# Optimization experiments

Measured on AMD Instinct MI355X. Metric: run time of the kernel, lower is better.

Reference implementation:

```python
import jax, jax.numpy as jnp
import numpy as np

N = 100000          # nodes
E = 3200000         # edges (avg degree 32)
D_IN = 64           # node_feature_dim
D_EMB = 128         # config.GNN_EMBEDDING_DIM
D_HID = 256         # config.RNN_HIDDEN_DIM


def setup_inputs() -> dict:
    key = jax.random.key(0)
    ks = jax.random.split(key, 12)
    s = 0.05
    return {
        "node_features": jax.random.normal(ks[0], (N, D_IN), jnp.float32),
        "edge_attr": jax.random.normal(ks[1], (E, 1), jnp.float32),
        "hidden_state": jax.random.normal(ks[2], (1, D_HID), jnp.float32),
        "W_enc": jax.random.normal(ks[3], (D_EMB, D_IN), jnp.float32) * s,
        "b_enc": jnp.zeros((D_EMB,), jnp.float32),
        "W_gcn": jax.random.normal(ks[4], (D_EMB, D_EMB), jnp.float32) * s,
        "b_gcn": jnp.zeros((D_EMB,), jnp.float32),
        "W_ih": jax.random.normal(ks[5], (3 * D_HID, D_EMB), jnp.float32) * s,
        "W_hh": jax.random.normal(ks[6], (3 * D_HID, D_HID), jnp.float32) * s,
        "b_ih": jax.random.normal(ks[7], (3 * D_HID,), jnp.float32) * s,
        "b_hh": jax.random.normal(ks[8], (3 * D_HID,), jnp.float32) * s,
        "edge_index": jax.random.randint(ks[9], (2, E), 0, N, jnp.int64),
    }


def reference(node_features, edge_attr, hidden_state, W_enc, b_enc, W_gcn,
              b_gcn, W_ih, W_hh, b_ih, b_hh, edge_index):
    n = node_features.shape[0]
    # Linear encoder + ReLU
    x = jax.nn.relu(node_features @ W_enc.T + b_enc)
    # GCNConv (PyG default): x' = D^-1/2 (A+I) D^-1/2 (x W^T) + b
    xw = x @ W_gcn.T
    loops = jnp.arange(n, dtype=edge_index.dtype)
    src = jnp.concatenate([edge_index[0], loops])
    dst = jnp.concatenate([edge_index[1], loops])
    deg = jax.ops.segment_sum(jnp.ones(src.shape, xw.dtype), dst, num_segments=n)
    dinv = jnp.where(deg > 0, jax.lax.rsqrt(deg), 0.0)
    norm = dinv[src] * dinv[dst]  # [E+N]
    agg = jax.ops.segment_sum(norm[:, None] * xw[src], dst, num_segments=n)
    g = jax.nn.relu(agg + b_gcn)
    agent = g[0:1, :]  # [1, D_EMB]
    # GRUCell
    gi = agent @ W_ih.T + b_ih
    gh = hidden_state @ W_hh.T + b_hh
    i_r, i_z, i_n = jnp.split(gi, 3, axis=1)
    h_r, h_z, h_n = jnp.split(gh, 3, axis=1)
    r = jax.nn.sigmoid(i_r + h_r)
    z = jax.nn.sigmoid(i_z + h_z)
    nn_ = jnp.tanh(i_n + r * h_n)
    return (1.0 - z) * nn_ + z * hidden_state
```

## Files before the change

kernel.cpp:

```cpp
#include <hip/hip_runtime.h>
#include <hip/hip_bf16.h>
#include <cstddef>

typedef __hip_bfloat16 bf16;

#define SB   1024
#define SL   32
#define CAP  256
#define TILE 64

__device__ __forceinline__ float ldf(const void* p, int isf32, long long i) {
    if (isf32) return ((const float*)p)[i];
    return __bfloat162float(((const bf16*)p)[i]);
}

__device__ __forceinline__ void detect(const void* ei, const void* wenc,
                                       int& is64, int& isf32) {
    int l = threadIdx.x & 63;
    int hi = (l < 16) ? ((const int*)ei)[2 * l + 1] : 0;
    unsigned long long any_hi = __ballot(hi != 0);
    unsigned short u = ((const unsigned short*)wenc)[l];
    unsigned short ex = (u >> 7) & 0xFF;
    unsigned long long any_big = __ballot(ex >= 137);
    is64  = (any_hi == 0ull) ? 1 : 0;
    isf32 = (any_big != 0ull) ? 1 : 0;
}

__device__ __forceinline__ void build_list(const int* __restrict__ cnts,
                                           const int* __restrict__ srcs,
                                           int* ls_src, int* ls_slot,
                                           int* sh_cnt, int* sh_tot,
                                           int& cnt, int& tot) {
    const int t = threadIdx.x;
    if (t == 0) { *sh_cnt = 0; *sh_tot = 0; }
    __syncthreads();
    for (int i = t; i < SB; i += 256) {
        int c = cnts[i];
        if (c > 0) {
            atomicAdd(sh_tot, c);
            int cc = min(c, SL);
            int base = atomicAdd(sh_cnt, cc);
            for (int j = 0; j < cc; j++) {
                int pos = base + j;
                if (pos < CAP) {
                    ls_src[pos]  = srcs[i * SL + j];
                    ls_slot[pos] = i * SL + j;
                }
            }
        }
    }
    __syncthreads();
    cnt = min(*sh_cnt, CAP);
    tot = *sh_tot;
}

__global__ void __launch_bounds__(256) k_scan(
        const void* __restrict__ ei, long long E,
        const void* __restrict__ wenc,
        const void* __restrict__ hid,
        const void* __restrict__ Whh, const void* __restrict__ bhh,
        int* __restrict__ cnts, int* __restrict__ srcs,
        int* __restrict__ degs, float* __restrict__ gh) {
    __shared__ float red[4];
    __shared__ int lc;
    __shared__ int ls[SL];
    int is64, isf32;
    detect(ei, wenc, is64, isf32);
    const int b = blockIdx.x;
    const int t = threadIdx.x;
    if (b < SB) {
        if (t == 0) lc = 0;
        if (t < SL) degs[b * SL + t] = 0;
        __syncthreads();
        const long long NT = (long long)SB * 256;
        if ((E & 1) == 0) {
            const long long P = E >> 1;
            for (long long p = (long long)b * 256 + t; p < P; p += NT) {
                int d0, d1;
                if (is64) {
                    longlong2 dd = ((const longlong2*)ei)[P + p];
                    d0 = (int)dd.x; d1 = (int)dd.y;
                } else {
                    int2 dd = ((const int2*)ei)[P + p];
                    d0 = dd.x; d1 = dd.y;
                }
                if (d0 == 0) {
                    int q = atomicAdd(&lc, 1);
                    if (q < SL) ls[q] = (int)(is64 ? ((const long long*)ei)[2*p]
                                                   : (long long)((const int*)ei)[2*p]);
                }
                if (d1 == 0) {
                    int q = atomicAdd(&lc, 1);
                    if (q < SL) ls[q] = (int)(is64 ? ((const long long*)ei)[2*p+1]
                                                   : (long long)((const int*)ei)[2*p+1]);
                }
            }
        } else {
            for (long long e = (long long)b * 256 + t; e < E; e += NT) {
                int d = is64 ? (int)((const long long*)ei)[E + e] : ((const int*)ei)[E + e];
                if (d == 0) {
                    int q = atomicAdd(&lc, 1);
                    if (q < SL) ls[q] = (int)(is64 ? ((const long long*)ei)[e]
                                                   : (long long)((const int*)ei)[e]);
                }
            }
        }
        __syncthreads();
        int c = lc;
        if (t == 0) cnts[b] = c;
        if (t < min(c, SL)) srcs[b * SL + t] = ls[t];
    } else {
        int j = b - SB;
        float p = ldf(Whh, isf32, (long long)j * 256 + t) * ldf(hid, isf32, t);
        #pragma unroll
        for (int off = 32; off > 0; off >>= 1) p += __shfl_down(p, off);
        if ((t & 63) == 0) red[t >> 6] = p;
        __syncthreads();
        if (t == 0) gh[j] = red[0] + red[1] + red[2] + red[3] + ldf(bhh, isf32, j);
    }
}

__global__ void __launch_bounds__(256) k_deg(
        const void* __restrict__ ei, long long E,
        const void* __restrict__ wenc,
        const int* __restrict__ cnts, const int* __restrict__ srcs,
        int* __restrict__ degs) {
    __shared__ int ls_src[CAP];
    __shared__ int ls_slot[CAP];
    __shared__ int sh_cnt, sh_tot;
    int is64, isf32;
    detect(ei, wenc, is64, isf32);
    (void)isf32;
    int cnt, tot;
    build_list(cnts, srcs, ls_src, ls_slot, &sh_cnt, &sh_tot, cnt, tot);
    const int b = blockIdx.x;
    const int t = threadIdx.x;
    const long long NT = (long long)gridDim.x * 256;
    if ((E & 1) == 0) {
        const long long P = E >> 1;
        for (long long p = (long long)b * 256 + t; p < P; p += NT) {
            int d0, d1;
            if (is64) {
                longlong2 dd = ((const longlong2*)ei)[P + p];
                d0 = (int)dd.x; d1 = (int)dd.y;
            } else {
                int2 dd = ((const int2*)ei)[P + p];
                d0 = dd.x; d1 = dd.y;
            }
            for (int j = 0; j < cnt; j++) {
                if (ls_src[j] == d0) atomicAdd(&degs[ls_slot[j]], 1);
                if (ls_src[j] == d1) atomicAdd(&degs[ls_slot[j]], 1);
            }
        }
    } else {
        for (long long e = (long long)b * 256 + t; e < E; e += NT) {
            int d = is64 ? (int)((const long long*)ei)[E + e] : ((const int*)ei)[E + e];
            for (int j = 0; j < cnt; j++)
                if (ls_src[j] == d) atomicAdd(&degs[ls_slot[j]], 1);
        }
    }
}

__global__ void __launch_bounds__(256) k_gru(
        const void* __restrict__ ei,
        const void* __restrict__ nf,
        const void* __restrict__ Wenc, const void* __restrict__ benc,
        const void* __restrict__ Wgcn, const void* __restrict__ bgcn,
        const void* __restrict__ hid,
        const void* __restrict__ Wih,  const void* __restrict__ bih,
        const int* __restrict__ cnts, const int* __restrict__ srcs,
        const int* __restrict__ degs, const float* __restrict__ gh,
        void* __restrict__ out) {
    __shared__ int   ls_src[CAP];
    __shared__ int   ls_slot[CAP];
    __shared__ int   sh_cnt, sh_tot;
    __shared__ float norm_s[CAP + 1];
    __shared__ __align__(16) float xs[TILE][64];
    __shared__ float part[2][128];
    __shared__ float ysum_s[128];
    __shared__ float g0_s[128];
    __shared__ float red[3];
    int is64, isf32;
    detect(ei, Wenc, is64, isf32);
    (void)is64;
    int cnt, tot;
    build_list(cnts, srcs, ls_src, ls_slot, &sh_cnt, &sh_tot, cnt, tot);
    const int t = threadIdx.x;
    const int lane = t & 63, wid = t >> 6;
    const int td = t & 127, hf = t >> 7;

    const int deg0 = tot + 1;
    const float r0 = rsqrtf((float)deg0);
    for (int i = t; i < cnt; i += 256)
        norm_s[i] = rsqrtf((float)(degs[ls_slot[i]] + 1)) * r0;
    if (t == 0) norm_s[cnt] = 1.0f / (float)deg0;
    const int total = cnt + 1;

    float4 wreg[16];
    if (isf32) {
        const float4* wr = (const float4*)((const float*)Wenc + (size_t)td * 64);
        #pragma unroll
        for (int k = 0; k < 16; k++) wreg[k] = wr[k];
    }
    const float be = ldf(benc, isf32, td);
    float ysum_acc = 0.0f;
    __syncthreads();

    for (int base = 0; base < total; base += TILE) {
        const int tn = min(TILE, total - base);
        for (int idx = t; idx < tn * 64; idx += 256) {
            int j = idx >> 6, c = idx & 63;
            int node = base + j;
            int s = (node < cnt) ? ls_src[node] : 0;
            xs[j][c] = ldf(nf, isf32, (long long)s * 64 + c);
        }
        __syncthreads();
        if (isf32) {
            for (int jj = hf; jj < tn; jj += 4) {
                const int ok2 = (jj + 2 < tn);
                const float4* xa = (const float4*)xs[jj];
                const float4* xb = (const float4*)xs[ok2 ? jj + 2 : jj];
                float aa = 0.0f, ab = 0.0f;
                #pragma unroll
                for (int k = 0; k < 16; k++) {
                    float4 va = xa[k], vb = xb[k], w = wreg[k];
                    aa += w.x*va.x + w.y*va.y + w.z*va.z + w.w*va.w;
                    ab += w.x*vb.x + w.y*vb.y + w.z*vb.z + w.w*vb.w;
                }
                float ya = fmaxf(aa + be, 0.0f);
                float yb = fmaxf(ab + be, 0.0f);
                ysum_acc += norm_s[base + jj] * ya
                          + (ok2 ? norm_s[base + jj + 2] * yb : 0.0f);
            }
        } else {
            for (int j = hf; j < tn; j += 2) {
                float acc = 0.0f;
                for (int k = 0; k < 64; k++)
                    acc += ldf(Wenc, 0, (long long)td * 64 + k) * xs[j][k];
                ysum_acc += norm_s[base + j] * fmaxf(acc + be, 0.0f);
            }
        }
        __syncthreads();
    }
    part[hf][td] = ysum_acc;
    __syncthreads();
    if (t < 128) ysum_s[t] = part[0][t] + part[1][t];
    __syncthreads();

    {
        float acc = 0.0f;
        if (isf32) {
            const float4* gr = (const float4*)((const float*)Wgcn
                                + (size_t)td * 128 + (size_t)hf * 64);
            const float* ys = ysum_s + hf * 64;
            #pragma unroll
            for (int k = 0; k < 16; k++) {
                float4 v = gr[k];
                acc += v.x*ys[4*k] + v.y*ys[4*k+1] + v.z*ys[4*k+2] + v.w*ys[4*k+3];
            }
        } else {
            for (int k = 0; k < 64; k++)
                acc += ldf(Wgcn, 0, (long long)td * 128 + hf * 64 + k)
                     * ysum_s[hf * 64 + k];
        }
        part[hf][td] = acc;
    }
    __syncthreads();
    if (t < 128)
        g0_s[t] = fmaxf(part[0][t] + part[1][t] + ldf(bgcn, isf32, t), 0.0f);
    __syncthreads();

    const int b = blockIdx.x;
    if (wid < 3) {
        long long j = (long long)wid * 256 + b;
        float a;
        if (isf32) {
            const float* wr = (const float*)Wih + (size_t)j * 128;
            a = wr[lane] * g0_s[lane] + wr[64 + lane] * g0_s[64 + lane];
        } else {
            a = ldf(Wih, 0, j * 128 + lane)      * g0_s[lane]
              + ldf(Wih, 0, j * 128 + 64 + lane) * g0_s[64 + lane];
        }
        #pragma unroll
        for (int off = 32; off > 0; off >>= 1) a += __shfl_down(a, off);
        if (lane == 0) red[wid] = a;
    }
    __syncthreads();
    if (t == 0) {
        float rr = 1.0f / (1.0f + expf(-(red[0] + ldf(bih, isf32, b)       + gh[b])));
        float zz = 1.0f / (1.0f + expf(-(red[1] + ldf(bih, isf32, 256 + b) + gh[256 + b])));
        float nn = tanhf(red[2] + ldf(bih, isf32, 512 + b) + rr * gh[512 + b]);
        float hh = ldf(hid, isf32, b);
        float val = (1.0f - zz) * nn + zz * hh;
        if (isf32) ((float*)out)[b] = val;
        else       ((bf16*)out)[b]  = __float2bfloat16(val);
    }
}

extern "C" void kernel_launch(void* const* d_in, const int* in_sizes, int n_in,
                              void* d_out, int out_size, void* d_ws, size_t ws_size,
                              hipStream_t stream) {
    const void* nf   = d_in[0];
    const void* hid  = d_in[2];
    const void* Wenc = d_in[3];
    const void* benc = d_in[4];
    const void* Wgcn = d_in[5];
    const void* bgcn = d_in[6];
    const void* Wih  = d_in[7];
    const void* Whh  = d_in[8];
    const void* bih  = d_in[9];
    const void* bhh  = d_in[10];
    const void* ei   = d_in[11];
    long long E = in_sizes[11] / 2;

    int*   cnts = (int*)d_ws;
    int*   srcs = cnts + SB;
    int*   degs = srcs + SB * SL;
    float* gh   = (float*)(degs + SB * SL);

    k_scan<<<SB + 768, 256, 0, stream>>>(ei, E, Wenc, hid, Whh, bhh,
                                         cnts, srcs, degs, gh);
    k_deg<<<2048, 256, 0, stream>>>(ei, E, Wenc, cnts, srcs, degs);
    k_gru<<<256, 256, 0, stream>>>(ei, nf, Wenc, benc, Wgcn, bgcn, hid,
                                   Wih, bih, cnts, srcs, degs, gh, d_out);
}
```

Before: 146.2 us.

## Prefetch weights and neighbour features into cache, move W_hh GEMV into GRU kernel

Adds prefetch blocks to the scan kernel that read all weight matrices so they sit in L2/MALL before the final kernel needs them. Adds an extra block to the degree kernel that touches node-0's neighbour feature rows for the same reason. Moves the hidden-state GEMV from the scan kernel into the GRU kernel and doubles the scan grid. This shortens the latency-bound last kernel, at the cost of extra blocks and redundant loads in the earlier kernels.

```diff
diff --git a/kernel.cpp b/kernel.cpp
--- a/kernel.cpp
+++ b/kernel.cpp
@@ -4,7 +4,8 @@
 
 typedef __hip_bfloat16 bf16;
 
-#define SB   1024
+#define SB   2048
+#define WB   64
 #define SL   32
 #define CAP  256
 #define TILE 64
@@ -56,86 +57,100 @@
 
 __global__ void __launch_bounds__(256) k_scan(
         const void* __restrict__ ei, long long E,
-        const void* __restrict__ wenc,
-        const void* __restrict__ hid,
-        const void* __restrict__ Whh, const void* __restrict__ bhh,
+        const void* __restrict__ Wenc,
+        const void* __restrict__ Wgcn,
+        const void* __restrict__ Wih, const void* __restrict__ Whh,
         int* __restrict__ cnts, int* __restrict__ srcs,
-        int* __restrict__ degs, float* __restrict__ gh) {
-    __shared__ float red[4];
+        int* __restrict__ degs) {
     __shared__ int lc;
     __shared__ int ls[SL];
     int is64, isf32;
-    detect(ei, wenc, is64, isf32);
+    detect(ei, Wenc, is64, isf32);
     const int b = blockIdx.x;
     const int t = threadIdx.x;
-    if (b < SB) {
-        if (t == 0) lc = 0;
-        if (t < SL) degs[b * SL + t] = 0;
-        __syncthreads();
-        const long long NT = (long long)SB * 256;
-        if ((E & 1) == 0) {
-            const long long P = E >> 1;
-            for (long long p = (long long)b * 256 + t; p < P; p += NT) {
-                int d0, d1;
-                if (is64) {
-                    longlong2 dd = ((const longlong2*)ei)[P + p];
-                    d0 = (int)dd.x; d1 = (int)dd.y;
-                } else {
-                    int2 dd = ((const int2*)ei)[P + p];
-                    d0 = dd.x; d1 = dd.y;
-                }
-                if (d0 == 0) {
-                    int q = atomicAdd(&lc, 1);
-                    if (q < SL) ls[q] = (int)(is64 ? ((const long long*)ei)[2*p]
-                                                   : (long long)((const int*)ei)[2*p]);
-                }
-                if (d1 == 0) {
-                    int q = atomicAdd(&lc, 1);
-                    if (q < SL) ls[q] = (int)(is64 ? ((const long long*)ei)[2*p+1]
-                                                   : (long long)((const int*)ei)[2*p+1]);
-                }
-            }
-        } else {
-            for (long long e = (long long)b * 256 + t; e < E; e += NT) {
-                int d = is64 ? (int)((const long long*)ei)[E + e] : ((const int*)ei)[E + e];
-                if (d == 0) {
-                    int q = atomicAdd(&lc, 1);
-                    if (q < SL) ls[q] = (int)(is64 ? ((const long long*)ei)[e]
-                                                   : (long long)((const int*)ei)[e]);
-                }
-            }
-        }
-        __syncthreads();
-        int c = lc;
-        if (t == 0) cnts[b] = c;
-        if (t < min(c, SL)) srcs[b * SL + t] = ls[t];
+    if (b < WB) {
+        const long long esz = isf32 ? 4 : 2;
+        const void* arrs[4]  = { Wenc, Wgcn, Wih, Whh };
+        const long long el[4] = { 128 * 64, 128 * 128, 768 * 128, 768 * 256 };
+        int acc = 0;
+        for (int a = 0; a < 4; a++) {
+            const char* pb = (const char*)arrs[a];
+            const long long nb = el[a] * esz;
+            for (long long off = ((long long)b * 256 + t) * 16;
+                 off + 16 <= nb; off += (long long)WB * 256 * 16) {
+                int4 v = *(const int4*)(pb + off);
+                acc += v.x + v.y + v.z + v.w;
+            }
+        }
+        asm volatile("" :: "v"(acc));
+        return;
+    }
+    const int sb = b - WB;
+    if (t == 0) lc = 0;
+    if (t < SL) degs[sb * SL + t] = 0;
+    __syncthreads();
+    const long long NT = (long long)SB * 256;
+    if ((E & 1) == 0) {
+        const long long P = E >> 1;
+        for (long long p = (long long)sb * 256 + t; p < P; p += NT) {
+            int d0, d1;
+            if (is64) {
+                longlong2 dd = ((const longlong2*)ei)[P + p];
+                d0 = (int)dd.x; d1 = (int)dd.y;
+            } else {
+                int2 dd = ((const int2*)ei)[P + p];
+                d0 = dd.x; d1 = dd.y;
+            }
+            if (d0 == 0) {
+                int q = atomicAdd(&lc, 1);
+                if (q < SL) ls[q] = (int)(is64 ? ((const long long*)ei)[2*p]
+                                               : (long long)((const int*)ei)[2*p]);
+            }
+            if (d1 == 0) {
+                int q = atomicAdd(&lc, 1);
+                if (q < SL) ls[q] = (int)(is64 ? ((const long long*)ei)[2*p+1]
+                                               : (long long)((const int*)ei)[2*p+1]);
+            }
+        }
     } else {
-        int j = b - SB;
-        float p = ldf(Whh, isf32, (long long)j * 256 + t) * ldf(hid, isf32, t);
-        #pragma unroll
-        for (int off = 32; off > 0; off >>= 1) p += __shfl_down(p, off);
-        if ((t & 63) == 0) red[t >> 6] = p;
-        __syncthreads();
-        if (t == 0) gh[j] = red[0] + red[1] + red[2] + red[3] + ldf(bhh, isf32, j);
-    }
+        for (long long e = (long long)sb * 256 + t; e < E; e += NT) {
+            int d = is64 ? (int)((const long long*)ei)[E + e] : ((const int*)ei)[E + e];
+            if (d == 0) {
+                int q = atomicAdd(&lc, 1);
+                if (q < SL) ls[q] = (int)(is64 ? ((const long long*)ei)[e]
+                                               : (long long)((const int*)ei)[e]);
+            }
+        }
+    }
+    __syncthreads();
+    int c = lc;
+    if (t == 0) cnts[sb] = c;
+    if (t < min(c, SL)) srcs[sb * SL + t] = ls[t];
 }
 
 __global__ void __launch_bounds__(256) k_deg(
         const void* __restrict__ ei, long long E,
         const void* __restrict__ wenc,
+        const void* __restrict__ nf,
         const int* __restrict__ cnts, const int* __restrict__ srcs,
-        int* __restrict__ degs) {
+        int* __restrict__ degs, int DB) {
     __shared__ int ls_src[CAP];
     __shared__ int ls_slot[CAP];
     __shared__ int sh_cnt, sh_tot;
     int is64, isf32;
     detect(ei, wenc, is64, isf32);
-    (void)isf32;
     int cnt, tot;
     build_list(cnts, srcs, ls_src, ls_slot, &sh_cnt, &sh_tot, cnt, tot);
     const int b = blockIdx.x;
     const int t = threadIdx.x;
-    const long long NT = (long long)gridDim.x * 256;
+    if (b >= DB) {
+        float s = 0.0f;
+        for (int idx = t; idx < cnt * 64; idx += 256)
+            s += ldf(nf, isf32, (long long)ls_src[idx >> 6] * 64 + (idx & 63));
+        asm volatile("" :: "v"(s));
+        return;
+    }
+    const long long NT = (long long)DB * 256;
     if ((E & 1) == 0) {
         const long long P = E >> 1;
         for (long long p = (long long)b * 256 + t; p < P; p += NT) {
@@ -168,18 +183,19 @@
         const void* __restrict__ Wgcn, const void* __restrict__ bgcn,
         const void* __restrict__ hid,
         const void* __restrict__ Wih,  const void* __restrict__ bih,
+        const void* __restrict__ Whh,  const void* __restrict__ bhh,
         const int* __restrict__ cnts, const int* __restrict__ srcs,
-        const int* __restrict__ degs, const float* __restrict__ gh,
-        void* __restrict__ out) {
+        const int* __restrict__ degs, void* __restrict__ out) {
     __shared__ int   ls_src[CAP];
     __shared__ int   ls_slot[CAP];
     __shared__ int   sh_cnt, sh_tot;
     __shared__ float norm_s[CAP + 1];
+    __shared__ float hid_s[256];
     __shared__ __align__(16) float xs[TILE][64];
     __shared__ float part[2][128];
     __shared__ float ysum_s[128];
     __shared__ float g0_s[128];
-    __shared__ float red[3];
+    __shared__ float red_ih[3], red_hh[3];
     int is64, isf32;
     detect(ei, Wenc, is64, isf32);
     (void)is64;
@@ -188,6 +204,7 @@
     const int t = threadIdx.x;
     const int lane = t & 63, wid = t >> 6;
     const int td = t & 127, hf = t >> 7;
+    hid_s[t] = ldf(hid, isf32, t);
 
     const int deg0 = tot + 1;
     const float r0 = rsqrtf((float)deg0);
@@ -273,24 +290,37 @@
     const int b = blockIdx.x;
     if (wid < 3) {
         long long j = (long long)wid * 256 + b;
-        float a;
+        float aih, ahh = 0.0f;
         if (isf32) {
             const float* wr = (const float*)Wih + (size_t)j * 128;
-            a = wr[lane] * g0_s[lane] + wr[64 + lane] * g0_s[64 + lane];
+            aih = wr[lane] * g0_s[lane] + wr[64 + lane] * g0_s[64 + lane];
+            const float* hr = (const float*)Whh + (size_t)j * 256;
+            #pragma unroll
+            for (int q = 0; q < 4; q++)
+                ahh += hr[q * 64 + lane] * hid_s[q * 64 + lane];
         } else {
-            a = ldf(Wih, 0, j * 128 + lane)      * g0_s[lane]
-              + ldf(Wih, 0, j * 128 + 64 + lane) * g0_s[64 + lane];
+            aih = ldf(Wih, 0, j * 128 + lane)      * g0_s[lane]
+                + ldf(Wih, 0, j * 128 + 64 + lane) * g0_s[64 + lane];
+            #pragma unroll
+            for (int q = 0; q < 4; q++)
+                ahh += ldf(Whh, 0, j * 256 + q * 64 + lane) * hid_s[q * 64 + lane];
         }
         #pragma unroll
-        for (int off = 32; off > 0; off >>= 1) a += __shfl_down(a, off);
-        if (lane == 0) red[wid] = a;
+        for (int off = 32; off > 0; off >>= 1) {
+            aih += __shfl_down(aih, off);
+            ahh += __shfl_down(ahh, off);
+        }
+        if (lane == 0) { red_ih[wid] = aih; red_hh[wid] = ahh; }
     }
     __syncthreads();
     if (t == 0) {
-        float rr = 1.0f / (1.0f + expf(-(red[0] + ldf(bih, isf32, b)       + gh[b])));
-        float zz = 1.0f / (1.0f + expf(-(red[1] + ldf(bih, isf32, 256 + b) + gh[256 + b])));
-        float nn = tanhf(red[2] + ldf(bih, isf32, 512 + b) + rr * gh[512 + b]);
-        float hh = ldf(hid, isf32, b);
+        float gh0 = red_hh[0] + ldf(bhh, isf32, b);
+        float gh1 = red_hh[1] + ldf(bhh, isf32, 256 + b);
+        float gh2 = red_hh[2] + ldf(bhh, isf32, 512 + b);
+        float rr = 1.0f / (1.0f + expf(-(red_ih[0] + ldf(bih, isf32, b)       + gh0)));
+        float zz = 1.0f / (1.0f + expf(-(red_ih[1] + ldf(bih, isf32, 256 + b) + gh1)));
+        float nn = tanhf(red_ih[2] + ldf(bih, isf32, 512 + b) + rr * gh2);
+        float hh = hid_s[b];
         float val = (1.0f - zz) * nn + zz * hh;
         if (isf32) ((float*)out)[b] = val;
         else       ((bf16*)out)[b]  = __float2bfloat16(val);
@@ -313,14 +343,14 @@
     const void* ei   = d_in[11];
     long long E = in_sizes[11] / 2;
 
-    int*   cnts = (int*)d_ws;
-    int*   srcs = cnts + SB;
-    int*   degs = srcs + SB * SL;
-    float* gh   = (float*)(degs + SB * SL);
-
-    k_scan<<<SB + 768, 256, 0, stream>>>(ei, E, Wenc, hid, Whh, bhh,
-                                         cnts, srcs, degs, gh);
-    k_deg<<<2048, 256, 0, stream>>>(ei, E, Wenc, cnts, srcs, degs);
+    int* cnts = (int*)d_ws;
+    int* srcs = cnts + SB;
+    int* degs = srcs + SB * SL;
+
+    const int DB = 2048;
+    k_scan<<<WB + SB, 256, 0, stream>>>(ei, E, Wenc, Wgcn, Wih, Whh,
+                                        cnts, srcs, degs);
+    k_deg<<<DB + 1, 256, 0, stream>>>(ei, E, Wenc, nf, cnts, srcs, degs, DB);
     k_gru<<<256, 256, 0, stream>>>(ei, nf, Wenc, benc, Wgcn, bgcn, hid,
-                                   Wih, bih, cnts, srcs, degs, gh, d_out);
-}
+                                   Wih, bih, Whh, bhh, cnts, srcs, degs, d_out);
+}
```

Measured after the change: 153.8 us. 1.05x slower.

## Fuse scan, degree and GRU stages into one cooperative persistent kernel

Applied to the files above, without the earlier changes.

Replaces the three-kernel pipeline with a single cooperative kernel. Each block scans the destination indices once, keeps them in registers, and uses global atomic counters with spin-wait barriers to publish agent-neighbor lists and their degrees before the first GRU blocks run the gather and GRU step. The W_hh matvec moves into the GRU blocks, and the original three-kernel path is kept as a fallback if the cooperative launch fails. This removes launch gaps and the second full read of the edge list, at the cost of grid-wide spin barriers and an occupancy-limited grid size.

```diff
diff --git a/kernel.cpp b/kernel.cpp
--- a/kernel.cpp
+++ b/kernel.cpp
@@ -4,10 +4,14 @@
 
 typedef __hip_bfloat16 bf16;
 
-#define SB   1024
-#define SL   32
-#define CAP  256
-#define TILE 64
+#define CAP   256
+#define PMAX  16
+#define GRUB  256
+#define SL    32
+#define TILE  64
+#define SB3   1024
+#define DB3   2048
+#define MAGIC 0x9E3779B1
 
 __device__ __forceinline__ float ldf(const void* p, int isf32, long long i) {
     if (isf32) return ((const float*)p)[i];
@@ -26,176 +30,38 @@
     isf32 = (any_big != 0ull) ? 1 : 0;
 }
 
-__device__ __forceinline__ void build_list(const int* __restrict__ cnts,
-                                           const int* __restrict__ srcs,
-                                           int* ls_src, int* ls_slot,
-                                           int* sh_cnt, int* sh_tot,
-                                           int& cnt, int& tot) {
-    const int t = threadIdx.x;
-    if (t == 0) { *sh_cnt = 0; *sh_tot = 0; }
-    __syncthreads();
-    for (int i = t; i < SB; i += 256) {
-        int c = cnts[i];
-        if (c > 0) {
-            atomicAdd(sh_tot, c);
-            int cc = min(c, SL);
-            int base = atomicAdd(sh_cnt, cc);
-            for (int j = 0; j < cc; j++) {
-                int pos = base + j;
-                if (pos < CAP) {
-                    ls_src[pos]  = srcs[i * SL + j];
-                    ls_slot[pos] = i * SL + j;
-                }
-            }
-        }
-    }
-    __syncthreads();
-    cnt = min(*sh_cnt, CAP);
-    tot = *sh_tot;
-}
-
-__global__ void __launch_bounds__(256) k_scan(
-        const void* __restrict__ ei, long long E,
-        const void* __restrict__ wenc,
-        const void* __restrict__ hid,
-        const void* __restrict__ Whh, const void* __restrict__ bhh,
-        int* __restrict__ cnts, int* __restrict__ srcs,
-        int* __restrict__ degs, float* __restrict__ gh) {
-    __shared__ float red[4];
-    __shared__ int lc;
-    __shared__ int ls[SL];
-    int is64, isf32;
-    detect(ei, wenc, is64, isf32);
-    const int b = blockIdx.x;
-    const int t = threadIdx.x;
-    if (b < SB) {
-        if (t == 0) lc = 0;
-        if (t < SL) degs[b * SL + t] = 0;
-        __syncthreads();
-        const long long NT = (long long)SB * 256;
-        if ((E & 1) == 0) {
-            const long long P = E >> 1;
-            for (long long p = (long long)b * 256 + t; p < P; p += NT) {
-                int d0, d1;
-                if (is64) {
-                    longlong2 dd = ((const longlong2*)ei)[P + p];
-                    d0 = (int)dd.x; d1 = (int)dd.y;
-                } else {
-                    int2 dd = ((const int2*)ei)[P + p];
-                    d0 = dd.x; d1 = dd.y;
-                }
-                if (d0 == 0) {
-                    int q = atomicAdd(&lc, 1);
-                    if (q < SL) ls[q] = (int)(is64 ? ((const long long*)ei)[2*p]
-                                                   : (long long)((const int*)ei)[2*p]);
-                }
-                if (d1 == 0) {
-                    int q = atomicAdd(&lc, 1);
-                    if (q < SL) ls[q] = (int)(is64 ? ((const long long*)ei)[2*p+1]
-                                                   : (long long)((const int*)ei)[2*p+1]);
-                }
-            }
-        } else {
-            for (long long e = (long long)b * 256 + t; e < E; e += NT) {
-                int d = is64 ? (int)((const long long*)ei)[E + e] : ((const int*)ei)[E + e];
-                if (d == 0) {
-                    int q = atomicAdd(&lc, 1);
-                    if (q < SL) ls[q] = (int)(is64 ? ((const long long*)ei)[e]
-                                                   : (long long)((const int*)ei)[e]);
-                }
-            }
-        }
-        __syncthreads();
-        int c = lc;
-        if (t == 0) cnts[b] = c;
-        if (t < min(c, SL)) srcs[b * SL + t] = ls[t];
-    } else {
-        int j = b - SB;
-        float p = ldf(Whh, isf32, (long long)j * 256 + t) * ldf(hid, isf32, t);
-        #pragma unroll
-        for (int off = 32; off > 0; off >>= 1) p += __shfl_down(p, off);
-        if ((t & 63) == 0) red[t >> 6] = p;
-        __syncthreads();
-        if (t == 0) gh[j] = red[0] + red[1] + red[2] + red[3] + ldf(bhh, isf32, j);
-    }
-}
-
-__global__ void __launch_bounds__(256) k_deg(
-        const void* __restrict__ ei, long long E,
-        const void* __restrict__ wenc,
-        const int* __restrict__ cnts, const int* __restrict__ srcs,
-        int* __restrict__ degs) {
-    __shared__ int ls_src[CAP];
-    __shared__ int ls_slot[CAP];
-    __shared__ int sh_cnt, sh_tot;
-    int is64, isf32;
-    detect(ei, wenc, is64, isf32);
-    (void)isf32;
-    int cnt, tot;
-    build_list(cnts, srcs, ls_src, ls_slot, &sh_cnt, &sh_tot, cnt, tot);
-    const int b = blockIdx.x;
-    const int t = threadIdx.x;
-    const long long NT = (long long)gridDim.x * 256;
-    if ((E & 1) == 0) {
-        const long long P = E >> 1;
-        for (long long p = (long long)b * 256 + t; p < P; p += NT) {
-            int d0, d1;
-            if (is64) {
-                longlong2 dd = ((const longlong2*)ei)[P + p];
-                d0 = (int)dd.x; d1 = (int)dd.y;
-            } else {
-                int2 dd = ((const int2*)ei)[P + p];
-                d0 = dd.x; d1 = dd.y;
-            }
-            for (int j = 0; j < cnt; j++) {
-                if (ls_src[j] == d0) atomicAdd(&degs[ls_slot[j]], 1);
-                if (ls_src[j] == d1) atomicAdd(&degs[ls_slot[j]], 1);
-            }
-        }
-    } else {
-        for (long long e = (long long)b * 256 + t; e < E; e += NT) {
-            int d = is64 ? (int)((const long long*)ei)[E + e] : ((const int*)ei)[E + e];
-            for (int j = 0; j < cnt; j++)
-                if (ls_src[j] == d) atomicAdd(&degs[ls_slot[j]], 1);
-        }
-    }
-}
-
-__global__ void __launch_bounds__(256) k_gru(
-        const void* __restrict__ ei,
+__device__ __forceinline__ int aload(int* p) {
+    return __hip_atomic_load(p, __ATOMIC_RELAXED, __HIP_MEMORY_SCOPE_AGENT);
+}
+__device__ __forceinline__ void backoff() {
+    #pragma unroll
+    for (int i = 0; i < 8; i++) __builtin_amdgcn_s_sleep(7);
+}
+
+struct GruSmem {
+    float norm_s[CAP + 1];
+    float hid_s[256];
+    __align__(16) float xs[TILE][64];
+    float part[2][128];
+    float ysum_s[128];
+    float g0_s[128];
+    float red_ih[3], red_hh[3];
+};
+
+__device__ __forceinline__ void gather_gru(
+        const int* __restrict__ ls_src, GruSmem* sm, int cnt, int isf32, int ob,
         const void* __restrict__ nf,
         const void* __restrict__ Wenc, const void* __restrict__ benc,
         const void* __restrict__ Wgcn, const void* __restrict__ bgcn,
         const void* __restrict__ hid,
         const void* __restrict__ Wih,  const void* __restrict__ bih,
-        const int* __restrict__ cnts, const int* __restrict__ srcs,
-        const int* __restrict__ degs, const float* __restrict__ gh,
+        const void* __restrict__ Whh,  const void* __restrict__ bhh,
         void* __restrict__ out) {
-    __shared__ int   ls_src[CAP];
-    __shared__ int   ls_slot[CAP];
-    __shared__ int   sh_cnt, sh_tot;
-    __shared__ float norm_s[CAP + 1];
-    __shared__ __align__(16) float xs[TILE][64];
-    __shared__ float part[2][128];
-    __shared__ float ysum_s[128];
-    __shared__ float g0_s[128];
-    __shared__ float red[3];
-    int is64, isf32;
-    detect(ei, Wenc, is64, isf32);
-    (void)is64;
-    int cnt, tot;
-    build_list(cnts, srcs, ls_src, ls_slot, &sh_cnt, &sh_tot, cnt, tot);
     const int t = threadIdx.x;
     const int lane = t & 63, wid = t >> 6;
     const int td = t & 127, hf = t >> 7;
-
-    const int deg0 = tot + 1;
-    const float r0 = rsqrtf((float)deg0);
-    for (int i = t; i < cnt; i += 256)
-        norm_s[i] = rsqrtf((float)(degs[ls_slot[i]] + 1)) * r0;
-    if (t == 0) norm_s[cnt] = 1.0f / (float)deg0;
+    sm->hid_s[t] = ldf(hid, isf32, t);
     const int total = cnt + 1;
-
     float4 wreg[16];
     if (isf32) {
         const float4* wr = (const float4*)((const float*)Wenc + (size_t)td * 64);
@@ -205,21 +71,20 @@
     const float be = ldf(benc, isf32, td);
     float ysum_acc = 0.0f;
     __syncthreads();
-
     for (int base = 0; base < total; base += TILE) {
         const int tn = min(TILE, total - base);
         for (int idx = t; idx < tn * 64; idx += 256) {
             int j = idx >> 6, c = idx & 63;
             int node = base + j;
             int s = (node < cnt) ? ls_src[node] : 0;
-            xs[j][c] = ldf(nf, isf32, (long long)s * 64 + c);
+            sm->xs[j][c] = ldf(nf, isf32, (long long)s * 64 + c);
         }
         __syncthreads();
         if (isf32) {
             for (int jj = hf; jj < tn; jj += 4) {
                 const int ok2 = (jj + 2 < tn);
-                const float4* xa = (const float4*)xs[jj];
-                const float4* xb = (const float4*)xs[ok2 ? jj + 2 : jj];
+                const float4* xa = (const float4*)sm->xs[jj];
+                const float4* xb = (const float4*)sm->xs[ok2 ? jj + 2 : jj];
                 float aa = 0.0f, ab = 0.0f;
                 #pragma unroll
                 for (int k = 0; k < 16; k++) {
@@ -229,30 +94,29 @@
                 }
                 float ya = fmaxf(aa + be, 0.0f);
                 float yb = fmaxf(ab + be, 0.0f);
-                ysum_acc += norm_s[base + jj] * ya
-                          + (ok2 ? norm_s[base + jj + 2] * yb : 0.0f);
+                ysum_acc += sm->norm_s[base + jj] * ya
+                          + (ok2 ? sm->norm_s[base + jj + 2] * yb : 0.0f);
             }
         } else {
             for (int j = hf; j < tn; j += 2) {
                 float acc = 0.0f;
                 for (int k = 0; k < 64; k++)
-                    acc += ldf(Wenc, 0, (long long)td * 64 + k) * xs[j][k];
-                ysum_acc += norm_s[base + j] * fmaxf(acc + be, 0.0f);
+                    acc += ldf(Wenc, 0, (long long)td * 64 + k) * sm->xs[j][k];
+                ysum_acc += sm->norm_s[base + j] * fmaxf(acc + be, 0.0f);
             }
         }
         __syncthreads();
     }
-    part[hf][td] = ysum_acc;
-    __syncthreads();
-    if (t < 128) ysum_s[t] = part[0][t] + part[1][t];
-    __syncthreads();
-
+    sm->part[hf][td] = ysum_acc;
+    __syncthreads();
+    if (t < 128) sm->ysum_s[t] = sm->part[0][t] + sm->part[1][t];
+    __syncthreads();
     {
         float acc = 0.0f;
         if (isf32) {
             const float4* gr = (const float4*)((const float*)Wgcn
                                 + (size_t)td * 128 + (size_t)hf * 64);
-            const float* ys = ysum_s + hf * 64;
+            const float* ys = sm->ysum_s + hf * 64;
             #pragma unroll
             for (int k = 0; k < 16; k++) {
                 float4 v = gr[k];
@@ -261,40 +125,343 @@
         } else {
             for (int k = 0; k < 64; k++)
                 acc += ldf(Wgcn, 0, (long long)td * 128 + hf * 64 + k)
-                     * ysum_s[hf * 64 + k];
-        }
-        part[hf][td] = acc;
+                     * sm->ysum_s[hf * 64 + k];
+        }
+        sm->part[hf][td] = acc;
     }
     __syncthreads();
     if (t < 128)
-        g0_s[t] = fmaxf(part[0][t] + part[1][t] + ldf(bgcn, isf32, t), 0.0f);
-    __syncthreads();
-
-    const int b = blockIdx.x;
+        sm->g0_s[t] = fmaxf(sm->part[0][t] + sm->part[1][t]
+                            + ldf(bgcn, isf32, t), 0.0f);
+    __syncthreads();
     if (wid < 3) {
-        long long j = (long long)wid * 256 + b;
-        float a;
+        long long j = (long long)wid * 256 + ob;
+        float aih, ahh = 0.0f;
         if (isf32) {
             const float* wr = (const float*)Wih + (size_t)j * 128;
-            a = wr[lane] * g0_s[lane] + wr[64 + lane] * g0_s[64 + lane];
+            aih = wr[lane] * sm->g0_s[lane] + wr[64 + lane] * sm->g0_s[64 + lane];
+            const float* hr = (const float*)Whh + (size_t)j * 256;
+            #pragma unroll
+            for (int q = 0; q < 4; q++)
+                ahh += hr[q * 64 + lane] * sm->hid_s[q * 64 + lane];
         } else {
-            a = ldf(Wih, 0, j * 128 + lane)      * g0_s[lane]
-              + ldf(Wih, 0, j * 128 + 64 + lane) * g0_s[64 + lane];
+            aih = ldf(Wih, 0, j * 128 + lane)      * sm->g0_s[lane]
+                + ldf(Wih, 0, j * 128 + 64 + lane) * sm->g0_s[64 + lane];
+            #pragma unroll
+            for (int q = 0; q < 4; q++)
+                ahh += ldf(Whh, 0, j * 256 + q * 64 + lane) * sm->hid_s[q * 64 + lane];
         }
         #pragma unroll
-        for (int off = 32; off > 0; off >>= 1) a += __shfl_down(a, off);
-        if (lane == 0) red[wid] = a;
+        for (int off = 32; off > 0; off >>= 1) {
+            aih += __shfl_down(aih, off);
+            ahh += __shfl_down(ahh, off);
+        }
+        if (lane == 0) { sm->red_ih[wid] = aih; sm->red_hh[wid] = ahh; }
     }
     __syncthreads();
     if (t == 0) {
-        float rr = 1.0f / (1.0f + expf(-(red[0] + ldf(bih, isf32, b)       + gh[b])));
-        float zz = 1.0f / (1.0f + expf(-(red[1] + ldf(bih, isf32, 256 + b) + gh[256 + b])));
-        float nn = tanhf(red[2] + ldf(bih, isf32, 512 + b) + rr * gh[512 + b]);
-        float hh = ldf(hid, isf32, b);
+        float gh0 = sm->red_hh[0] + ldf(bhh, isf32, ob);
+        float gh1 = sm->red_hh[1] + ldf(bhh, isf32, 256 + ob);
+        float gh2 = sm->red_hh[2] + ldf(bhh, isf32, 512 + ob);
+        float rr = 1.0f / (1.0f + expf(-(sm->red_ih[0] + ldf(bih, isf32, ob)       + gh0)));
+        float zz = 1.0f / (1.0f + expf(-(sm->red_ih[1] + ldf(bih, isf32, 256 + ob) + gh1)));
+        float nn = tanhf(sm->red_ih[2] + ldf(bih, isf32, 512 + ob) + rr * gh2);
+        float hh = sm->hid_s[ob];
         float val = (1.0f - zz) * nn + zz * hh;
-        if (isf32) ((float*)out)[b] = val;
-        else       ((bf16*)out)[b]  = __float2bfloat16(val);
-    }
+        if (isf32) ((float*)out)[ob] = val;
+        else       ((bf16*)out)[ob]  = __float2bfloat16(val);
+    }
+}
+
+__global__ void __launch_bounds__(256, 2) k_one(
+        const void* __restrict__ ei, long long E,
+        const void* __restrict__ nf,
+        const void* __restrict__ Wenc, const void* __restrict__ benc,
+        const void* __restrict__ Wgcn, const void* __restrict__ bgcn,
+        const void* __restrict__ hid,
+        const void* __restrict__ Wih,  const void* __restrict__ bih,
+        const void* __restrict__ Whh,  const void* __restrict__ bhh,
+        int* __restrict__ hdr, int* __restrict__ degs_g, int* __restrict__ srcs_g,
+        void* __restrict__ out) {
+    __shared__ int lc;
+    __shared__ int lsv[SL];
+    __shared__ int sbase;
+    __shared__ int ls_src[CAP];
+    __shared__ int sh_cnt, sh_tot;
+    __shared__ GruSmem sm;
+
+    int is64, isf32;
+    detect(ei, Wenc, is64, isf32);
+    const int b = blockIdx.x, t = threadIdx.x;
+    const int G = (int)gridDim.x;
+
+    if (t == 0) lc = 0;
+    if (b == 0) {
+        if (t < 64) hdr[t] = 0;
+        degs_g[t] = 0;
+        __threadfence();
+    }
+    __syncthreads();
+    if (b == 0 && t == 0) atomicExch(&hdr[48], MAGIC);
+
+    int rd[2 * PMAX];
+    #pragma unroll
+    for (int r = 0; r < 2 * PMAX; r++) rd[r] = -1;
+    const long long stride = (long long)G * 256;
+    const long long i0 = (long long)b * 256 + t;
+    if ((E & 1) == 0) {
+        const long long P = E >> 1;
+        #pragma unroll
+        for (int r = 0; r < PMAX; r++) {
+            long long p = i0 + (long long)r * stride;
+            if (p < P) {
+                int d0, d1;
+                if (is64) { longlong2 dd = ((const longlong2*)ei)[P + p];
+                            d0 = (int)dd.x; d1 = (int)dd.y; }
+                else      { int2 dd = ((const int2*)ei)[P + p];
+                            d0 = dd.x; d1 = dd.y; }
+                rd[2*r] = d0; rd[2*r+1] = d1;
+                if (d0 == 0) { int q = atomicAdd(&lc, 1);
+                    if (q < SL) lsv[q] = (int)(is64 ? ((const long long*)ei)[2*p]
+                                                    : (long long)((const int*)ei)[2*p]); }
+                if (d1 == 0) { int q = atomicAdd(&lc, 1);
+                    if (q < SL) lsv[q] = (int)(is64 ? ((const long long*)ei)[2*p+1]
+                                                    : (long long)((const int*)ei)[2*p+1]); }
+            }
+        }
+        for (long long p = i0 + (long long)PMAX * stride; p < P; p += stride) {
+            int d0, d1;
+            if (is64) { longlong2 dd = ((const longlong2*)ei)[P + p];
+                        d0 = (int)dd.x; d1 = (int)dd.y; }
+            else      { int2 dd = ((const int2*)ei)[P + p];
+                        d0 = dd.x; d1 = dd.y; }
+            if (d0 == 0) { int q = atomicAdd(&lc, 1);
+                if (q < SL) lsv[q] = (int)(is64 ? ((const long long*)ei)[2*p]
+                                                : (long long)((const int*)ei)[2*p]); }
+            if (d1 == 0) { int q = atomicAdd(&lc, 1);
+                if (q < SL) lsv[q] = (int)(is64 ? ((const long long*)ei)[2*p+1]
+                                                : (long long)((const int*)ei)[2*p+1]); }
+        }
+    } else {
+        #pragma unroll
+        for (int r = 0; r < 2 * PMAX; r++) {
+            long long e = i0 + (long long)r * stride;
+            if (e < E) {
+                int d = is64 ? (int)((const long long*)ei)[E + e]
+                             : ((const int*)ei)[E + e];
+                rd[r] = d;
+                if (d == 0) { int q = atomicAdd(&lc, 1);
+                    if (q < SL) lsv[q] = (int)(is64 ? ((const long long*)ei)[e]
+                                                    : (long long)((const int*)ei)[e]); }
+            }
+        }
+        for (long long e = i0 + (long long)(2 * PMAX) * stride; e < E; e += stride) {
+            int d = is64 ? (int)((const long long*)ei)[E + e] : ((const int*)ei)[E + e];
+            if (d == 0) { int q = atomicAdd(&lc, 1);
+                if (q < SL) lsv[q] = (int)(is64 ? ((const long long*)ei)[e]
+                                                : (long long)((const int*)ei)[e]); }
+        }
+    }
+
+    __syncthreads();
+    if (t == 0) {
+        while (aload(&hdr[48]) != MAGIC) backoff();
+        int c = lc;
+        if (c > 0) {
+            atomicAdd(&hdr[0], c);
+            sbase = atomicAdd(&hdr[8], min(c, SL));
+        } else sbase = 0;
+    }
+    __syncthreads();
+    {
+        int cc = min(lc, SL);
+        if (t < cc) { int pos = sbase + t;
+                      if (pos < CAP) atomicExch(&srcs_g[pos], lsv[t]); }
+    }
+    __syncthreads();
+    __threadfence();
+    if (t == 0) {
+        atomicAdd(&hdr[16], 1);
+        while (aload(&hdr[16]) < G) backoff();
+        sh_cnt = min(aload(&hdr[8]), CAP);
+        sh_tot = aload(&hdr[0]);
+    }
+    __syncthreads();
+    __threadfence();
+    const int cnt = sh_cnt;
+    if (t < cnt) ls_src[t] = aload(&srcs_g[t]);
+    __syncthreads();
+
+    for (int j = 0; j < cnt; j++) {
+        int sj = ls_src[j];
+        int m = 0;
+        #pragma unroll
+        for (int r = 0; r < 2 * PMAX; r++) m += (rd[r] == sj) ? 1 : 0;
+        if (m) atomicAdd(&degs_g[j], m);
+    }
+    if ((E & 1) == 0) {
+        const long long P = E >> 1;
+        for (long long p = i0 + (long long)PMAX * stride; p < P; p += stride) {
+            int d0, d1;
+            if (is64) { longlong2 dd = ((const longlong2*)ei)[P + p];
+                        d0 = (int)dd.x; d1 = (int)dd.y; }
+            else      { int2 dd = ((const int2*)ei)[P + p];
+                        d0 = dd.x; d1 = dd.y; }
+            for (int j = 0; j < cnt; j++) {
+                if (ls_src[j] == d0) atomicAdd(&degs_g[j], 1);
+                if (ls_src[j] == d1) atomicAdd(&degs_g[j], 1);
+            }
+        }
+    } else {
+        for (long long e = i0 + (long long)(2 * PMAX) * stride; e < E; e += stride) {
+            int d = is64 ? (int)((const long long*)ei)[E + e] : ((const int*)ei)[E + e];
+            for (int j = 0; j < cnt; j++)
+                if (ls_src[j] == d) atomicAdd(&degs_g[j], 1);
+        }
+    }
+    __syncthreads();
+    __threadfence();
+    if (t == 0) atomicAdd(&hdr[32], 1);
+    if (b >= GRUB) return;
+    if (t == 0) { while (aload(&hdr[32]) < G) backoff(); }
+    __syncthreads();
+    __threadfence();
+
+    const int tot = sh_tot;
+    const float r0 = rsqrtf((float)(tot + 1));
+    if (t < cnt)
+        sm.norm_s[t] = rsqrtf((float)(aload(&degs_g[t]) + 1)) * r0;
+    if (t == 255) sm.norm_s[cnt] = 1.0f / (float)(tot + 1);
+    gather_gru(ls_src, &sm, cnt, isf32, b, nf, Wenc, benc, Wgcn, bgcn,
+               hid, Wih, bih, Whh, bhh, out);
+}
+
+__device__ __forceinline__ void build_list(const int* __restrict__ cnts,
+                                           const int* __restrict__ srcs, int sbN,
+                                           int* ls_src, int* ls_slot,
+                                           int* sh_cnt, int* sh_tot,
+                                           int& cnt, int& tot) {
+    const int t = threadIdx.x;
+    if (t == 0) { *sh_cnt = 0; *sh_tot = 0; }
+    __syncthreads();
+    for (int i = t; i < sbN; i += 256) {
+        int c = cnts[i];
+        if (c > 0) {
+            atomicAdd(sh_tot, c);
+            int cc = min(c, SL);
+            int base = atomicAdd(sh_cnt, cc);
+            for (int j = 0; j < cc; j++) {
+                int pos = base + j;
+                if (pos < CAP) { ls_src[pos] = srcs[i * SL + j];
+                                 ls_slot[pos] = i * SL + j; }
+            }
+        }
+    }
+    __syncthreads();
+    cnt = min(*sh_cnt, CAP);
+    tot = *sh_tot;
+}
+
+__global__ void __launch_bounds__(256) k_scan_f(
+        const void* __restrict__ ei, long long E, const void* __restrict__ wenc,
+        int* __restrict__ cnts, int* __restrict__ srcs, int* __restrict__ degs) {
+    __shared__ int lc;
+    __shared__ int ls[SL];
+    int is64, isf32;
+    detect(ei, wenc, is64, isf32); (void)isf32;
+    const int b = blockIdx.x, t = threadIdx.x;
+    if (t == 0) lc = 0;
+    if (t < SL) degs[b * SL + t] = 0;
+    __syncthreads();
+    const long long NT = (long long)SB3 * 256;
+    if ((E & 1) == 0) {
+        const long long P = E >> 1;
+        for (long long p = (long long)b * 256 + t; p < P; p += NT) {
+            int d0, d1;
+            if (is64) { longlong2 dd = ((const longlong2*)ei)[P + p];
+                        d0 = (int)dd.x; d1 = (int)dd.y; }
+            else      { int2 dd = ((const int2*)ei)[P + p];
+                        d0 = dd.x; d1 = dd.y; }
+            if (d0 == 0) { int q = atomicAdd(&lc, 1);
+                if (q < SL) ls[q] = (int)(is64 ? ((const long long*)ei)[2*p]
+                                               : (long long)((const int*)ei)[2*p]); }
+            if (d1 == 0) { int q = atomicAdd(&lc, 1);
+                if (q < SL) ls[q] = (int)(is64 ? ((const long long*)ei)[2*p+1]
+                                               : (long long)((const int*)ei)[2*p+1]); }
+        }
+    } else {
+        for (long long e = (long long)b * 256 + t; e < E; e += NT) {
+            int d = is64 ? (int)((const long long*)ei)[E + e] : ((const int*)ei)[E + e];
+            if (d == 0) { int q = atomicAdd(&lc, 1);
+                if (q < SL) ls[q] = (int)(is64 ? ((const long long*)ei)[e]
+                                               : (long long)((const int*)ei)[e]); }
+        }
+    }
+    __syncthreads();
+    int c = lc;
+    if (t == 0) cnts[b] = c;
+    if (t < min(c, SL)) srcs[b * SL + t] = ls[t];
+}
+
+__global__ void __launch_bounds__(256) k_deg_f(
+        const void* __restrict__ ei, long long E, const void* __restrict__ wenc,
+        const int* __restrict__ cnts, const int* __restrict__ srcs,
+        int* __restrict__ degs) {
+    __shared__ int ls_src[CAP];
+    __shared__ int ls_slot[CAP];
+    __shared__ int sh_cnt, sh_tot;
+    int is64, isf32;
+    detect(ei, wenc, is64, isf32); (void)isf32;
+    int cnt, tot;
+    build_list(cnts, srcs, SB3, ls_src, ls_slot, &sh_cnt, &sh_tot, cnt, tot);
+    const int b = blockIdx.x, t = threadIdx.x;
+    const long long NT = (long long)gridDim.x * 256;
+    if ((E & 1) == 0) {
+        const long long P = E >> 1;
+        for (long long p = (long long)b * 256 + t; p < P; p += NT) {
+            int d0, d1;
+            if (is64) { longlong2 dd = ((const longlong2*)ei)[P + p];
+                        d0 = (int)dd.x; d1 = (int)dd.y; }
+            else      { int2 dd = ((const int2*)ei)[P + p];
+                        d0 = dd.x; d1 = dd.y; }
+            for (int j = 0; j < cnt; j++) {
+                if (ls_src[j] == d0) atomicAdd(&degs[ls_slot[j]], 1);
+                if (ls_src[j] == d1) atomicAdd(&degs[ls_slot[j]], 1);
+            }
+        }
+    } else {
+        for (long long e = (long long)b * 256 + t; e < E; e += NT) {
+            int d = is64 ? (int)((const long long*)ei)[E + e] : ((const int*)ei)[E + e];
+            for (int j = 0; j < cnt; j++)
+                if (ls_src[j] == d) atomicAdd(&degs[ls_slot[j]], 1);
+        }
+    }
+}
+
+__global__ void __launch_bounds__(256) k_gru_f(
+        const void* __restrict__ ei, const void* __restrict__ nf,
+        const void* __restrict__ Wenc, const void* __restrict__ benc,
+        const void* __restrict__ Wgcn, const void* __restrict__ bgcn,
+        const void* __restrict__ hid,
+        const void* __restrict__ Wih,  const void* __restrict__ bih,
+        const void* __restrict__ Whh,  const void* __restrict__ bhh,
+        const int* __restrict__ cnts, const int* __restrict__ srcs,
+        const int* __restrict__ degs, void* __restrict__ out) {
+    __shared__ int ls_src[CAP];
+    __shared__ int ls_slot[CAP];
+    __shared__ int sh_cnt, sh_tot;
+    __shared__ GruSmem sm;
+    int is64, isf32;
+    detect(ei, Wenc, is64, isf32); (void)is64;
+    int cnt, tot;
+    build_list(cnts, srcs, SB3, ls_src, ls_slot, &sh_cnt, &sh_tot, cnt, tot);
+    const int t = threadIdx.x;
+    const float r0 = rsqrtf((float)(tot + 1));
+    if (t < cnt)
+        sm.norm_s[t] = rsqrtf((float)(degs[ls_slot[t]] + 1)) * r0;
+    if (t == 255) sm.norm_s[cnt] = 1.0f / (float)(tot + 1);
+    gather_gru(ls_src, &sm, cnt, isf32, blockIdx.x, nf, Wenc, benc, Wgcn, bgcn,
+               hid, Wih, bih, Whh, bhh, out);
 }
 
 extern "C" void kernel_launch(void* const* d_in, const int* in_sizes, int n_in,
@@ -313,14 +480,43 @@
     const void* ei   = d_in[11];
     long long E = in_sizes[11] / 2;
 
-    int*   cnts = (int*)d_ws;
-    int*   srcs = cnts + SB;
-    int*   degs = srcs + SB * SL;
-    float* gh   = (float*)(degs + SB * SL);
-
-    k_scan<<<SB + 768, 256, 0, stream>>>(ei, E, Wenc, hid, Whh, bhh,
-                                         cnts, srcs, degs, gh);
-    k_deg<<<2048, 256, 0, stream>>>(ei, E, Wenc, cnts, srcs, degs);
-    k_gru<<<256, 256, 0, stream>>>(ei, nf, Wenc, benc, Wgcn, bgcn, hid,
-                                   Wih, bih, cnts, srcs, degs, gh, d_out);
-}
+    int* hdr    = (int*)d_ws;
+    int* degs_g = hdr + 64;
+    int* srcs_g = degs_g + CAP;
+    int* f_cnts = (int*)((char*)d_ws + 8192);
+    int* f_srcs = f_cnts + SB3;
+    int* f_degs = f_srcs + SB3 * SL;
+
+    static int g_total = 0;
+    if (g_total == 0) {
+        int bpc = 0;
+        if (hipOccupancyMaxActiveBlocksPerMultiprocessor(&bpc, k_one, 256, 0)
+                != hipSuccess || bpc < 1) bpc = 2;
+        int cus = 0, dev = 0;
+        hipDeviceProp_t prop;
+        if (hipGetDevice(&dev) == hipSuccess &&
+            hipGetDeviceProperties(&prop, dev) == hipSuccess)
+            cus = prop.multiProcessorCount;
+        if (cus <= 0) cus = 256;
+        long long tot = (long long)bpc * cus;
+        if (tot > 1024) tot = 1024;
+        if (tot < GRUB) tot = GRUB;
+        g_total = (int)tot;
+    }
+
+    void* outp = d_out;
+    void* args[] = { (void*)&ei, (void*)&E, (void*)&nf,
+                     (void*)&Wenc, (void*)&benc, (void*)&Wgcn, (void*)&bgcn,
+                     (void*)&hid, (void*)&Wih, (void*)&bih, (void*)&Whh,
+                     (void*)&bhh, (void*)&hdr, (void*)&degs_g, (void*)&srcs_g,
+                     (void*)&outp };
+    hipError_t err = hipLaunchCooperativeKernel((void*)k_one, dim3(g_total),
+                                                dim3(256), args, 0, stream);
+    if (err != hipSuccess) {
+        k_scan_f<<<SB3, 256, 0, stream>>>(ei, E, Wenc, f_cnts, f_srcs, f_degs);
+        k_deg_f<<<DB3, 256, 0, stream>>>(ei, E, Wenc, f_cnts, f_srcs, f_degs);
+        k_gru_f<<<GRUB, 256, 0, stream>>>(ei, nf, Wenc, benc, Wgcn, bgcn, hid,
+                                          Wih, bih, Whh, bhh,
+                                          f_cnts, f_srcs, f_degs, d_out);
+    }
+}
```

After: 281.2 us. 1.92x slower.
